# Optimization experiments

Hardware: AMD Instinct MI355X
Metric: run time of the kernel (lower is better)

The kernel has to match this reference:

```python
import jax, jax.numpy as jnp
import numpy as np

NUM_HEADS = 8

def setup_inputs() -> dict:
    key = jax.random.key(0)
    ks = jax.random.split(key, 5)
    B, L, D = 4, 2048, 512
    return {
        "query": jax.random.normal(ks[0], (B, L, D), jnp.float32),
        "key":   jax.random.normal(ks[1], (B, L, D), jnp.float32),
        "value": jax.random.normal(ks[2], (B, L, D), jnp.float32),
        "w_out": jax.random.normal(ks[3], (D, D), jnp.float32) * (1.0 / np.sqrt(D)),
        "b_out": jnp.zeros((D,), jnp.float32),
    }

def _scatter_rows(base, idx, vals):
    # base: [L, ...], idx: [u], vals: [u, ...]
    return base.at[idx].set(vals)

_scatter_bh = jax.vmap(jax.vmap(_scatter_rows))  # over (B, H)

def reference(query, key, value, w_out, b_out):
    B, L, D = query.shape
    H = NUM_HEADS
    hd = D // H
    scale = 1.0 / np.sqrt(hd)

    def split(x):
        return x.reshape(B, L, H, hd).transpose(0, 2, 1, 3)  # [B,H,L,hd]
    q, k, v = split(query), split(key), split(value)

    # dense scores for sparsity measure
    scores = jnp.einsum('bhld,bhmd->bhlm', q, k) * scale  # [B,H,L,L]
    m1 = jax.scipy.special.logsumexp(scores, axis=-1) - np.log(L).astype(np.float32)
    m2 = scores.mean(axis=-1)
    M_measure = m1 - m2  # [B,H,L]

    u = max(1, int(np.ceil(np.log(L + 1))))
    _, topk_idx = jax.lax.top_k(M_measure, u)  # [B,H,u]

    v_avg = v.mean(axis=2, keepdims=True)  # [B,H,1,hd]
    default_output = jnp.broadcast_to(v_avg, (B, H, L, hd))

    q_active = jnp.take_along_axis(q, topk_idx[..., None], axis=2)  # [B,H,u,hd]
    scores_active = jnp.einsum('bhud,bhmd->bhum', q_active, k) * scale  # [B,H,u,L]
    attn_weights_active = jax.nn.softmax(scores_active, axis=-1)  # dropout p=0
    attn_output_active = jnp.einsum('bhum,bhmd->bhud', attn_weights_active, v)  # [B,H,u,hd]

    attn_output = _scatter_bh(default_output, topk_idx, attn_output_active)  # [B,H,L,hd]
    attn_weights_full = _scatter_bh(
        jnp.zeros((B, H, L, L), scores.dtype), topk_idx, attn_weights_active)

    out = attn_output.transpose(0, 2, 1, 3).reshape(B, L, D)
    out = out @ w_out.T + b_out
    return out, attn_weights_full
```

## Files before the change

kernel.cpp:

```cpp
#include <hip/hip_runtime.h>
#include <hip/hip_bf16.h>

#define BB 4
#define LL 2048
#define DD 512
#define HH 8
#define HD 64
#define UU 8
#define BH (BB*HH)
#define SCALE 0.125f

typedef __attribute__((ext_vector_type(8))) short short8;
typedef __attribute__((ext_vector_type(4))) float f32x4;
typedef unsigned short ushortT;

#define GLDS(gp, lp) __builtin_amdgcn_global_load_lds( \
    (const __attribute__((address_space(1))) void*)(gp), \
    (__attribute__((address_space(3))) void*)(lp), 16, 0, 0)

__device__ __forceinline__ unsigned short bf16_rne(float x) {
    unsigned int u = __float_as_uint(x);
    unsigned int r = u + 0x7FFFu + ((u >> 16) & 1u);
    return (unsigned short)(r >> 16);
}

__global__ __launch_bounds__(256) void prep_fill(const float* __restrict__ Kin,
                                                 const float* __restrict__ Vin,
                                                 float* __restrict__ vsum_part,
                                                 float* __restrict__ ksum_part,
                                                 ushortT* __restrict__ KhiG,
                                                 ushortT* __restrict__ KloG,
                                                 f32x4* __restrict__ Wz,
                                                 int* __restrict__ map) {
    int t = threadIdx.x;
    if (blockIdx.x >= 1280) {
        int fid = blockIdx.x - 1280;
        const f32x4 z = {0.f, 0.f, 0.f, 0.f};
        size_t base = (size_t)fid*256 + t;
        const size_t stride = (size_t)8192*256;
        #pragma unroll
        for (int i = 0; i < 16; i++)
            Wz[base + (size_t)i*stride] = z;
        if (fid == 0) {
            #pragma unroll
            for (int j = 0; j < 32; j++) map[t + j*256] = 0;
        }
        return;
    }
    if (blockIdx.x < 256) {
        int blk = blockIdx.x;
        int bh = blk & 31, chunk = blk >> 5;
        int b = bh / HH, h = bh % HH;
        int d = t & 63; int g = t >> 6;
        const float* kb = Kin + (size_t)b*LL*DD + h*HD + d;
        const float* vb = Vin + (size_t)b*LL*DD + h*HD + d;
        float ak = 0.f, av = 0.f;
        for (int l = chunk*256 + g; l < chunk*256 + 256; l += 4) {
            ak += kb[(size_t)l*DD]; av += vb[(size_t)l*DD];
        }
        __shared__ float sk[4][64], sv[4][64];
        sk[g][d] = ak; sv[g][d] = av;
        __syncthreads();
        if (g == 0) {
            ksum_part[chunk*2048 + bh*64 + d] = sk[0][d]+sk[1][d]+sk[2][d]+sk[3][d];
            vsum_part[chunk*2048 + bh*64 + d] = sv[0][d]+sv[1][d]+sv[2][d]+sv[3][d];
        }
        return;
    }
    int blk = blockIdx.x - 256;
    int bh = blk >> 5, tile = blk & 31;
    int b = bh / HH, h = bh % HH;
    const float* kb = Kin + (size_t)b*LL*DD + h*HD;
    #pragma unroll
    for (int i = 0; i < 4; i++) {
        int f = t + i*256;
        int row = f >> 4, col4 = f & 15;
        float4 kv = *(const float4*)(kb + (size_t)(tile*64 + row)*DD + col4*4);
        float xs[4] = {kv.x, kv.y, kv.z, kv.w};
        unsigned short hb[4], lb[4];
        #pragma unroll
        for (int j = 0; j < 4; j++) {
            unsigned short hh = bf16_rne(xs[j]);
            float hf = __uint_as_float((unsigned int)hh << 16);
            hb[j] = hh; lb[j] = bf16_rne(xs[j] - hf);
        }
        int off = row*64 + (((col4>>1) ^ (row&7))<<3) + (col4&1)*4;
        uint2 uh; uh.x = hb[0] | ((unsigned)hb[1]<<16); uh.y = hb[2] | ((unsigned)hb[3]<<16);
        uint2 ul; ul.x = lb[0] | ((unsigned)lb[1]<<16); ul.y = lb[2] | ((unsigned)lb[3]<<16);
        *(uint2*)&KhiG[(size_t)blk*4096 + off] = uh;
        *(uint2*)&KloG[(size_t)blk*4096 + off] = ul;
    }
}

__global__ __launch_bounds__(256) void m_mfma(const float* __restrict__ Q,
                                              const ushortT* __restrict__ KhiG,
                                              const ushortT* __restrict__ KloG,
                                              const float* __restrict__ ksum_part,
                                              float* __restrict__ M) {
    int qt = blockIdx.x;
    int bh = blockIdx.y; int b = bh / HH, h = bh % HH;
    const int t = threadIdx.x;
    const int lane = t & 63, w = t >> 6;
    const int c = lane & 15, G = lane >> 4;

    __shared__ unsigned short kHi[2][4096];
    __shared__ unsigned short kLo[2][4096];
    __shared__ float ksLds[64];
    __shared__ float sm[128];

    const float* qb = Q + (size_t)b*LL*DD + h*HD;
    const char* khg = (const char*)(KhiG + (size_t)bh*32*4096);
    const char* klg = (const char*)(KloG + (size_t)bh*32*4096);

    short8 a_hi[2][2], a_lo[2][2];
    #pragma unroll
    for (int g = 0; g < 2; g++) {
        int qrow = qt*128 + w*32 + g*16 + c;
        const float* qr = qb + (size_t)qrow*DD + G*8;
        #pragma unroll
        for (int dh = 0; dh < 2; dh++) {
            float4 x0 = *(const float4*)(qr + dh*32);
            float4 x1 = *(const float4*)(qr + dh*32 + 4);
            float x[8] = {x0.x,x0.y,x0.z,x0.w, x1.x,x1.y,x1.z,x1.w};
            short8 hi, lo;
            #pragma unroll
            for (int j = 0; j < 8; j++) {
                float xs = x[j] * SCALE;
                unsigned short hb = bf16_rne(xs);
                float hf = __uint_as_float((unsigned int)hb << 16);
                hi[j] = (short)hb;
                lo[j] = (short)bf16_rne(xs - hf);
            }
            a_hi[g][dh] = hi; a_lo[g][dh] = lo;
        }
    }
    if (t < 64) {
        float s = 0.f;
        #pragma unroll
        for (int cc = 0; cc < 8; cc++) s += ksum_part[cc*2048 + bh*64 + t];
        ksLds[t] = s;
    }

    {
        char* dH = (char*)&kHi[0][0];
        char* dL = (char*)&kLo[0][0];
        unsigned o0 = w*1024, o1 = w*1024 + 4096;
        GLDS(khg + o0 + lane*16, dH + o0);
        GLDS(khg + o1 + lane*16, dH + o1);
        GLDS(klg + o0 + lane*16, dL + o0);
        GLDS(klg + o1 + lane*16, dL + o1);
    }
    float se[2][4] = {};
    __syncthreads();

    for (int r = 0; r < 32; r++) {
        int p = r & 1;
        if (r < 31) {
            const char* sH = khg + (size_t)(r+1)*8192;
            const char* sL = klg + (size_t)(r+1)*8192;
            char* dH = (char*)&kHi[p^1][0];
            char* dL = (char*)&kLo[p^1][0];
            unsigned o0 = w*1024, o1 = w*1024 + 4096;
            GLDS(sH + o0 + lane*16, dH + o0);
            GLDS(sH + o1 + lane*16, dH + o1);
            GLDS(sL + o0 + lane*16, dL + o0);
            GLDS(sL + o1 + lane*16, dL + o1);
        }
        #pragma unroll
        for (int kt = 0; kt < 4; kt++) {
            int rowIn = kt*16 + c;
            int sw = rowIn & 7;
            int base = rowIn*64;
            short8 bh0 = *(const short8*)&kHi[p][base + ((G       ^ sw)<<3)];
            short8 bh1 = *(const short8*)&kHi[p][base + (((G + 4) ^ sw)<<3)];
            short8 bl0 = *(const short8*)&kLo[p][base + ((G       ^ sw)<<3)];
            short8 bl1 = *(const short8*)&kLo[p][base + (((G + 4) ^ sw)<<3)];
            #pragma unroll
            for (int g = 0; g < 2; g++) {
                f32x4 acc = {0.f, 0.f, 0.f, 0.f};
                acc = __builtin_amdgcn_mfma_f32_16x16x32_bf16(a_hi[g][0], bh0, acc, 0, 0, 0);
                acc = __builtin_amdgcn_mfma_f32_16x16x32_bf16(a_hi[g][1], bh1, acc, 0, 0, 0);
                acc = __builtin_amdgcn_mfma_f32_16x16x32_bf16(a_lo[g][0], bh0, acc, 0, 0, 0);
                acc = __builtin_amdgcn_mfma_f32_16x16x32_bf16(a_lo[g][1], bh1, acc, 0, 0, 0);
                acc = __builtin_amdgcn_mfma_f32_16x16x32_bf16(a_hi[g][0], bl0, acc, 0, 0, 0);
                acc = __builtin_amdgcn_mfma_f32_16x16x32_bf16(a_hi[g][1], bl1, acc, 0, 0, 0);
                #pragma unroll
                for (int q4 = 0; q4 < 4; q4++) se[g][q4] += __expf(acc[q4]);
            }
        }
        __syncthreads();
    }

    #pragma unroll
    for (int g = 0; g < 2; g++)
        #pragma unroll
        for (int q4 = 0; q4 < 4; q4++) {
            float v = se[g][q4];
            v += __shfl_xor(v, 1);
            v += __shfl_xor(v, 2);
            v += __shfl_xor(v, 4);
            v += __shfl_xor(v, 8);
            se[g][q4] = v;
        }
    if (c == 0) {
        #pragma unroll
        for (int g = 0; g < 2; g++)
            #pragma unroll
            for (int q4 = 0; q4 < 4; q4++)
                sm[w*32 + g*16 + G*4 + q4] = se[g][q4];
    }
    __syncthreads();
    if (t < 128) {
        int qrow = qt*128 + t;
        const float* qr = qb + (size_t)qrow*DD;
        float dot = 0.f;
        for (int d0 = 0; d0 < 64; d0 += 4) {
            float4 qv = *(const float4*)(qr + d0);
            dot += qv.x*ksLds[d0] + qv.y*ksLds[d0+1] + qv.z*ksLds[d0+2] + qv.w*ksLds[d0+3];
        }
        M[bh*LL + qrow] = __logf(sm[t]) - __logf((float)LL) - dot * (SCALE/(float)LL);
    }
}

__global__ __launch_bounds__(256) void top8(const float* __restrict__ M,
                                            int* __restrict__ idx,
                                            int* __restrict__ map) {
    int bh = blockIdx.x; int t = threadIdx.x;
    __shared__ float Ml[LL];
    __shared__ float vals[256];
    __shared__ int   vidx[256];
    for (int i = t; i < LL; i += 256) Ml[i] = M[bh*LL + i];
    __syncthreads();
    for (int r = 0; r < UU; r++) {
        float bv = -1e30f; int bi = 0;
        for (int i = t; i < LL; i += 256) {
            float v = Ml[i];
            if (v > bv) { bv = v; bi = i; }
        }
        vals[t] = bv; vidx[t] = bi;
        __syncthreads();
        for (int s = 128; s > 0; s >>= 1) {
            if (t < s) {
                if (vals[t+s] > vals[t] ||
                    (vals[t+s] == vals[t] && vidx[t+s] < vidx[t])) {
                    vals[t] = vals[t+s]; vidx[t] = vidx[t+s];
                }
            }
            __syncthreads();
        }
        if (t == 0) {
            int w = vidx[0];
            idx[bh*UU + r] = w;
            Ml[w] = -1e30f;
            atomicOr(&map[(bh/HH)*LL + w], 1 << (bh % HH));
        }
        __syncthreads();
    }
}

__global__ __launch_bounds__(256) void active_attn(const float* __restrict__ Q,
                                                   const float* __restrict__ Kin,
                                                   const float* __restrict__ Vin,
                                                   const int* __restrict__ idx,
                                                   const float* __restrict__ vsum_part,
                                                   const float* __restrict__ w_out,
                                                   const float* __restrict__ b_out,
                                                   float* __restrict__ attn_o,
                                                   float* __restrict__ defo,
                                                   float* __restrict__ Wfull) {
    __shared__ float qs[64];
    __shared__ float w[LL];
    __shared__ float red[256];
    __shared__ float Kt[256][65];
    __shared__ float red4[16][16][4];
    int t = threadIdx.x;
    if (blockIdx.x >= BH*UU) {
        int b = blockIdx.x - BH*UU;
        for (int i = t; i < DD; i += 256) {
            float s = 0.f;
            #pragma unroll
            for (int cc = 0; cc < 8; cc++)
                s += vsum_part[cc*2048 + (b*HH + (i >> 6))*64 + (i & 63)];
            w[i] = s * (1.0f/LL);
        }
        __syncthreads();
        for (int dp = t; dp < DD; dp += 256) {
            const float* wr = w_out + (size_t)dp*DD;
            float acc = b_out[dp];
            for (int d0 = 0; d0 < DD; d0 += 4) {
                float4 wv = *(const float4*)(wr + d0);
                acc += w[d0]*wv.x + w[d0+1]*wv.y + w[d0+2]*wv.z + w[d0+3]*wv.w;
            }
            defo[b*DD + dp] = acc;
        }
        return;
    }
    int e = blockIdx.x;
    int bh = e / UU;
    int b = bh / HH, h = bh % HH;
    int l = idx[e];
    if (t < 64) qs[t] = Q[(size_t)b*LL*DD + (size_t)l*DD + h*HD + t];
    const float* kb = Kin + (size_t)b*LL*DD + h*HD;
    int srow = t >> 4, scol = t & 15;
    float4 nx[16];
    #pragma unroll
    for (int i = 0; i < 16; i++)
        nx[i] = *(const float4*)(kb + (size_t)(srow + i*16)*DD + scol*4);
    #pragma unroll
    for (int i = 0; i < 16; i++)
        *(float4*)&Kt[srow + i*16][scol*4] = nx[i];
    __syncthreads();

    float s[8];
    float mx = -1e30f;
    #pragma unroll
    for (int p = 0; p < 8; p++) {
        if (p < 7) {
            #pragma unroll
            for (int i = 0; i < 16; i++)
                nx[i] = *(const float4*)(kb + (size_t)((p+1)*256 + srow + i*16)*DD + scol*4);
        }
        float acc = 0.f;
        for (int d0 = 0; d0 < 64; d0 += 4) {
            acc += qs[d0]*Kt[t][d0] + qs[d0+1]*Kt[t][d0+1]
                 + qs[d0+2]*Kt[t][d0+2] + qs[d0+3]*Kt[t][d0+3];
        }
        s[p] = acc * SCALE;
        mx = fmaxf(mx, s[p]);
        __syncthreads();
        if (p < 7) {
            #pragma unroll
            for (int i = 0; i < 16; i++)
                *(float4*)&Kt[srow + i*16][scol*4] = nx[i];
        }
        __syncthreads();
    }
    red[t] = mx; __syncthreads();
    for (int st = 128; st > 0; st >>= 1) { if (t < st) red[t] = fmaxf(red[t], red[t+st]); __syncthreads(); }
    mx = red[0]; __syncthreads();
    float lsum = 0.f;
    #pragma unroll
    for (int p = 0; p < 8; p++) { s[p] = __expf(s[p] - mx); lsum += s[p]; }
    red[t] = lsum; __syncthreads();
    for (int st = 128; st > 0; st >>= 1) { if (t < st) red[t] += red[t+st]; __syncthreads(); }
    float inv = 1.0f / red[0]; __syncthreads();
    float* wrow = Wfull + ((size_t)bh*LL + l) * LL;
    #pragma unroll
    for (int p = 0; p < 8; p++) {
        int m = (p << 8) + t;
        float wn = s[p] * inv;
        w[m] = wn;
        wrow[m] = wn;
    }
    __syncthreads();
    const float4* vb4 = (const float4*)(Vin + (size_t)b*LL*DD + h*HD);
    int grp = t >> 4, d4 = t & 15;
    f32x4 acc = {0.f, 0.f, 0.f, 0.f};
    for (int it = 0; it < 128; it++) {
        int m = grp + it*16;
        float4 v4 = vb4[(size_t)m*128 + d4];
        float wm = w[m];
        acc[0] += wm * v4.x; acc[1] += wm * v4.y;
        acc[2] += wm * v4.z; acc[3] += wm * v4.w;
    }
    *(f32x4*)&red4[grp][d4][0] = acc;
    __syncthreads();
    if (t < 64) {
        int dq = t >> 2, comp = t & 3;
        float sum = 0.f;
        #pragma unroll
        for (int g = 0; g < 16; g++) sum += red4[g][dq][comp];
        attn_o[e*64 + t] = sum;
    }
}

__global__ __launch_bounds__(256) void out_kernel(const float* __restrict__ defo,
                                                  const float* __restrict__ vsum_part,
                                                  const float* __restrict__ attn_o,
                                                  const int* __restrict__ idx,
                                                  const int* __restrict__ map,
                                                  const float* __restrict__ w_out,
                                                  const float* __restrict__ b_out,
                                                  float* __restrict__ out) {
    int l = blockIdx.x, b = blockIdx.y;
    int t = threadIdx.x;
    float* orow = out + ((size_t)b*LL + l) * DD;
    int mp = map[b*LL + l];
    if (mp == 0) {
        const float* dr = defo + b*DD;
        orow[t] = dr[t]; orow[t + 256] = dr[t + 256];
        return;
    }
    __shared__ float x[DD];
    for (int i = t; i < DD; i += 256) {
        float s = 0.f;
        #pragma unroll
        for (int cc = 0; cc < 8; cc++)
            s += vsum_part[cc*2048 + (b*HH + (i >> 6))*64 + (i & 63)];
        x[i] = s * (1.0f/LL);
    }
    __syncthreads();
    if (t < 64) {
        for (int h = 0; h < HH; h++) if (mp & (1 << h)) {
            int bh = b*HH + h;
            int e = bh*UU;
            for (int j = 0; j < UU; j++) if (idx[bh*UU + j] == l) { e = bh*UU + j; break; }
            x[h*64 + t] = attn_o[e*64 + t];
        }
    }
    __syncthreads();
    for (int dp = t; dp < DD; dp += 256) {
        const float* wr = w_out + (size_t)dp*DD;
        float acc = b_out[dp];
        for (int d0 = 0; d0 < DD; d0 += 4) {
            float4 wv = *(const float4*)(wr + d0);
            acc += x[d0]*wv.x + x[d0+1]*wv.y + x[d0+2]*wv.z + x[d0+3]*wv.w;
        }
        orow[dp] = acc;
    }
}

extern "C" void kernel_launch(void* const* d_in, const int* in_sizes, int n_in,
                              void* d_out, int out_size, void* d_ws, size_t ws_size,
                              hipStream_t stream) {
    const float* Q     = (const float*)d_in[0];
    const float* Kin   = (const float*)d_in[1];
    const float* Vin   = (const float*)d_in[2];
    const float* w_out = (const float*)d_in[3];
    const float* b_out = (const float*)d_in[4];

    float* out   = (float*)d_out;
    float* Wfull = out + (size_t)BB*LL*DD;

    char* ws = (char*)d_ws;
    float*   vsum_part = (float*)(ws);
    float*   ksum_part = (float*)(ws + 65536);
    float*   M         = (float*)(ws + 131072);
    int*     idx       = (int*)  (ws + 393216);
    float*   attn_o    = (float*)(ws + 394240);
    int*     map       = (int*)  (ws + 459776);
    float*   defo      = (float*)(ws + 493568);
    ushortT* KhiG      = (ushortT*)(ws + (1u<<20));
    ushortT* KloG      = (ushortT*)(ws + (10u<<20));

    prep_fill<<<9472, 256, 0, stream>>>(Kin, Vin, vsum_part, ksum_part,
                                        KhiG, KloG, (f32x4*)Wfull, map);
    m_mfma<<<dim3(16, BH), 256, 0, stream>>>(Q, KhiG, KloG, ksum_part, M);
    top8<<<BH, 256, 0, stream>>>(M, idx, map);
    active_attn<<<BH*UU + BB, 256, 0, stream>>>(Q, Kin, Vin, idx, vsum_part, w_out, b_out,
                                                attn_o, defo, Wfull);
    out_kernel<<<dim3(LL, BB), 256, 0, stream>>>(defo, vsum_part, attn_o, idx, map, w_out, b_out, out);
}
```

Measured before the change: 425.3 us.

## Fuse top-k selection into score kernel via last-block election; use exp2 scaling

The separate top8 kernel is removed. The last m_mfma block to finish for each (batch, head) is chosen through an atomic counter with threadfences, and that block runs the top-k selection over M, reusing its K staging shared memory. This saves one kernel launch and its dependency gap, at the cost of atomics and a serial tail on the elected block. Q is also pre-scaled by scale*log2(e) so the exponentials use exp2f instead of __expf.

```diff
diff --git a/kernel.cpp b/kernel.cpp
--- a/kernel.cpp
+++ b/kernel.cpp
@@ -9,6 +9,7 @@
 #define UU 8
 #define BH (BB*HH)
 #define SCALE 0.125f
+#define ASCALE 0.18033688011112042f
 
 typedef __attribute__((ext_vector_type(8))) short short8;
 typedef __attribute__((ext_vector_type(4))) float f32x4;
@@ -31,7 +32,8 @@
                                                  ushortT* __restrict__ KhiG,
                                                  ushortT* __restrict__ KloG,
                                                  f32x4* __restrict__ Wz,
-                                                 int* __restrict__ map) {
+                                                 int* __restrict__ map,
+                                                 int* __restrict__ cnt) {
     int t = threadIdx.x;
     if (blockIdx.x >= 1280) {
         int fid = blockIdx.x - 1280;
@@ -44,6 +46,7 @@
         if (fid == 0) {
             #pragma unroll
             for (int j = 0; j < 32; j++) map[t + j*256] = 0;
+            if (t < 32) cnt[t] = 0;
         }
         return;
     }
@@ -96,7 +99,10 @@
                                               const ushortT* __restrict__ KhiG,
                                               const ushortT* __restrict__ KloG,
                                               const float* __restrict__ ksum_part,
-                                              float* __restrict__ M) {
+                                              float* __restrict__ M,
+                                              int* __restrict__ cnt,
+                                              int* __restrict__ idx,
+                                              int* __restrict__ map) {
     int qt = blockIdx.x;
     int bh = blockIdx.y; int b = bh / HH, h = bh % HH;
     const int t = threadIdx.x;
@@ -107,6 +113,7 @@
     __shared__ unsigned short kLo[2][4096];
     __shared__ float ksLds[64];
     __shared__ float sm[128];
+    __shared__ int elected;
 
     const float* qb = Q + (size_t)b*LL*DD + h*HD;
     const char* khg = (const char*)(KhiG + (size_t)bh*32*4096);
@@ -125,7 +132,7 @@
             short8 hi, lo;
             #pragma unroll
             for (int j = 0; j < 8; j++) {
-                float xs = x[j] * SCALE;
+                float xs = x[j] * ASCALE;
                 unsigned short hb = bf16_rne(xs);
                 float hf = __uint_as_float((unsigned int)hb << 16);
                 hi[j] = (short)hb;
@@ -185,7 +192,7 @@
                 acc = __builtin_amdgcn_mfma_f32_16x16x32_bf16(a_hi[g][0], bl0, acc, 0, 0, 0);
                 acc = __builtin_amdgcn_mfma_f32_16x16x32_bf16(a_hi[g][1], bl1, acc, 0, 0, 0);
                 #pragma unroll
-                for (int q4 = 0; q4 < 4; q4++) se[g][q4] += __expf(acc[q4]);
+                for (int q4 = 0; q4 < 4; q4++) se[g][q4] += exp2f(acc[q4]);
             }
         }
         __syncthreads();
@@ -220,18 +227,22 @@
         }
         M[bh*LL + qrow] = __logf(sm[t]) - __logf((float)LL) - dot * (SCALE/(float)LL);
     }
-}
-
-__global__ __launch_bounds__(256) void top8(const float* __restrict__ M,
-                                            int* __restrict__ idx,
-                                            int* __restrict__ map) {
-    int bh = blockIdx.x; int t = threadIdx.x;
-    __shared__ float Ml[LL];
-    __shared__ float vals[256];
-    __shared__ int   vidx[256];
-    for (int i = t; i < LL; i += 256) Ml[i] = M[bh*LL + i];
-    __syncthreads();
-    for (int r = 0; r < UU; r++) {
+
+    __threadfence();
+    if (t == 0) {
+        int old = atomicAdd(&cnt[bh], 1);
+        elected = (old == 15) ? 1 : 0;
+    }
+    __syncthreads();
+    if (!elected) return;
+    __threadfence();
+    float* Ml   = (float*)&kHi[0][0];
+    float* vals = (float*)&kLo[0][0];
+    int*   vidx = (int*)  &kLo[0][2048];
+    const volatile float* Mv = M + (size_t)bh*LL;
+    for (int i = t; i < LL; i += 256) Ml[i] = Mv[i];
+    __syncthreads();
+    for (int r2 = 0; r2 < UU; r2++) {
         float bv = -1e30f; int bi = 0;
         for (int i = t; i < LL; i += 256) {
             float v = Ml[i];
@@ -249,10 +260,10 @@
             __syncthreads();
         }
         if (t == 0) {
-            int w = vidx[0];
-            idx[bh*UU + r] = w;
-            Ml[w] = -1e30f;
-            atomicOr(&map[(bh/HH)*LL + w], 1 << (bh % HH));
+            int wi = vidx[0];
+            idx[bh*UU + r2] = wi;
+            Ml[wi] = -1e30f;
+            atomicOr(&map[(bh/HH)*LL + wi], 1 << (bh % HH));
         }
         __syncthreads();
     }
@@ -440,13 +451,13 @@
     float*   attn_o    = (float*)(ws + 394240);
     int*     map       = (int*)  (ws + 459776);
     float*   defo      = (float*)(ws + 493568);
+    int*     cnt       = (int*)  (ws + 501760);
     ushortT* KhiG      = (ushortT*)(ws + (1u<<20));
     ushortT* KloG      = (ushortT*)(ws + (10u<<20));
 
     prep_fill<<<9472, 256, 0, stream>>>(Kin, Vin, vsum_part, ksum_part,
-                                        KhiG, KloG, (f32x4*)Wfull, map);
-    m_mfma<<<dim3(16, BH), 256, 0, stream>>>(Q, KhiG, KloG, ksum_part, M);
-    top8<<<BH, 256, 0, stream>>>(M, idx, map);
+                                        KhiG, KloG, (f32x4*)Wfull, map, cnt);
+    m_mfma<<<dim3(16, BH), 256, 0, stream>>>(Q, KhiG, KloG, ksum_part, M, cnt, idx, map);
     active_attn<<<BH*UU + BB, 256, 0, stream>>>(Q, Kin, Vin, idx, vsum_part, w_out, b_out,
                                                 attn_o, defo, Wfull);
     out_kernel<<<dim3(LL, BB), 256, 0, stream>>>(defo, vsum_part, attn_o, idx, map, w_out, b_out, out);
```

After: 490.5 us. +15.3%, slower.

## Move attention-weight zero-fill into output kernel, skip active rows, use exp2

Applied to the files above, without the earlier changes.

The zero-fill of the 512 MB dense attention-weight tensor moves from the prep kernel into the output kernel. There it writes only rows not selected as active, so the rows active_attn writes are no longer written twice. This also shrinks the prep launch and puts the large store stream in a later kernel alongside the output writes. Separately, the query pre-scale now folds in log2(e) so the sparsity-measure exponentials use exp2f instead of __expf, which changes rounding slightly.

```diff
diff --git a/kernel.cpp b/kernel.cpp
--- a/kernel.cpp
+++ b/kernel.cpp
@@ -9,6 +9,7 @@
 #define UU 8
 #define BH (BB*HH)
 #define SCALE 0.125f
+#define ASCALE 0.18033688011112042f
 
 typedef __attribute__((ext_vector_type(8))) short short8;
 typedef __attribute__((ext_vector_type(4))) float f32x4;
@@ -24,31 +25,17 @@
     return (unsigned short)(r >> 16);
 }
 
-__global__ __launch_bounds__(256) void prep_fill(const float* __restrict__ Kin,
-                                                 const float* __restrict__ Vin,
-                                                 float* __restrict__ vsum_part,
-                                                 float* __restrict__ ksum_part,
-                                                 ushortT* __restrict__ KhiG,
-                                                 ushortT* __restrict__ KloG,
-                                                 f32x4* __restrict__ Wz,
-                                                 int* __restrict__ map) {
+__global__ __launch_bounds__(256) void prep(const float* __restrict__ Kin,
+                                            const float* __restrict__ Vin,
+                                            float* __restrict__ vsum_part,
+                                            float* __restrict__ ksum_part,
+                                            ushortT* __restrict__ KhiG,
+                                            ushortT* __restrict__ KloG,
+                                            int* __restrict__ map) {
     int t = threadIdx.x;
-    if (blockIdx.x >= 1280) {
-        int fid = blockIdx.x - 1280;
-        const f32x4 z = {0.f, 0.f, 0.f, 0.f};
-        size_t base = (size_t)fid*256 + t;
-        const size_t stride = (size_t)8192*256;
-        #pragma unroll
-        for (int i = 0; i < 16; i++)
-            Wz[base + (size_t)i*stride] = z;
-        if (fid == 0) {
-            #pragma unroll
-            for (int j = 0; j < 32; j++) map[t + j*256] = 0;
-        }
-        return;
-    }
     if (blockIdx.x < 256) {
         int blk = blockIdx.x;
+        if (blk < 32) map[blk*256 + t] = 0;
         int bh = blk & 31, chunk = blk >> 5;
         int b = bh / HH, h = bh % HH;
         int d = t & 63; int g = t >> 6;
@@ -125,7 +112,7 @@
             short8 hi, lo;
             #pragma unroll
             for (int j = 0; j < 8; j++) {
-                float xs = x[j] * SCALE;
+                float xs = x[j] * ASCALE;
                 unsigned short hb = bf16_rne(xs);
                 float hf = __uint_as_float((unsigned int)hb << 16);
                 hi[j] = (short)hb;
@@ -185,7 +172,7 @@
                 acc = __builtin_amdgcn_mfma_f32_16x16x32_bf16(a_hi[g][0], bl0, acc, 0, 0, 0);
                 acc = __builtin_amdgcn_mfma_f32_16x16x32_bf16(a_hi[g][1], bl1, acc, 0, 0, 0);
                 #pragma unroll
-                for (int q4 = 0; q4 < 4; q4++) se[g][q4] += __expf(acc[q4]);
+                for (int q4 = 0; q4 < 4; q4++) se[g][q4] += exp2f(acc[q4]);
             }
         }
         __syncthreads();
@@ -381,9 +368,28 @@
                                                   const int* __restrict__ map,
                                                   const float* __restrict__ w_out,
                                                   const float* __restrict__ b_out,
-                                                  float* __restrict__ out) {
+                                                  float* __restrict__ out,
+                                                  float* __restrict__ Wfull) {
     int l = blockIdx.x, b = blockIdx.y;
     int t = threadIdx.x;
+
+    {
+        int fid = b*LL + l;
+        f32x4* Wz = (f32x4*)Wfull;
+        const f32x4 z = {0.f, 0.f, 0.f, 0.f};
+        #pragma unroll
+        for (int rr = 0; rr < 8; rr++) {
+            int R = fid*8 + rr;
+            int bh2 = R >> 11, l2 = R & 2047;
+            int b2 = bh2 >> 3, h2 = bh2 & 7;
+            if (!((map[b2*LL + l2] >> h2) & 1)) {
+                f32x4* rowp = Wz + (size_t)R*512;
+                rowp[t] = z;
+                rowp[t + 256] = z;
+            }
+        }
+    }
+
     float* orow = out + ((size_t)b*LL + l) * DD;
     int mp = map[b*LL + l];
     if (mp == 0) {
@@ -443,11 +449,11 @@
     ushortT* KhiG      = (ushortT*)(ws + (1u<<20));
     ushortT* KloG      = (ushortT*)(ws + (10u<<20));
 
-    prep_fill<<<9472, 256, 0, stream>>>(Kin, Vin, vsum_part, ksum_part,
-                                        KhiG, KloG, (f32x4*)Wfull, map);
+    prep<<<1280, 256, 0, stream>>>(Kin, Vin, vsum_part, ksum_part, KhiG, KloG, map);
     m_mfma<<<dim3(16, BH), 256, 0, stream>>>(Q, KhiG, KloG, ksum_part, M);
     top8<<<BH, 256, 0, stream>>>(M, idx, map);
     active_attn<<<BH*UU + BB, 256, 0, stream>>>(Q, Kin, Vin, idx, vsum_part, w_out, b_out,
                                                 attn_o, defo, Wfull);
-    out_kernel<<<dim3(LL, BB), 256, 0, stream>>>(defo, vsum_part, attn_o, idx, map, w_out, b_out, out);
-}
+    out_kernel<<<dim3(LL, BB), 256, 0, stream>>>(defo, vsum_part, attn_o, idx, map,
+                                                 w_out, b_out, out, Wfull);
+}
```

Result: faster. 381.6 us (-10.3%).
